# Kernel tuning notes

Measured on AMD Instinct MI355X. Metric: run time of the kernel, lower is better.

## Reference

```python
import jax, jax.numpy as jnp
import numpy as np

N_P = 100000; N_F = 100000; N_PORT = 50000
F_IN = 64; H = 128; E = 200000; G = 128; OUT = 2


def setup_inputs() -> dict:
    key = jax.random.key(0)
    it = iter(jax.random.split(key, 64))
    def nrm(sh, s=1.0):
        return jax.random.normal(next(it), sh, jnp.float32) * s
    def ei(ns, nd):
        src = jax.random.randint(next(it), (E,), 0, ns)
        dst = jax.random.randint(next(it), (E,), 0, nd)
        return jnp.stack([src, dst]).astype(jnp.int32)
    def batch(n):
        return jnp.sort(jax.random.randint(next(it), (n,), 0, G)).astype(jnp.int32)
    return {
        'x_process': nrm((N_P, F_IN)), 'x_file': nrm((N_F, F_IN)), 'x_port': nrm((N_PORT, F_IN)),
        'W0': nrm((F_IN, H), 0.1), 'a0s': nrm((H,), 0.1), 'a0d': nrm((H,), 0.1), 'b0': jnp.zeros((H,), jnp.float32),
        'W1': nrm((H, H), 0.1), 'a1s': nrm((H,), 0.1), 'a1d': nrm((H,), 0.1), 'b1': jnp.zeros((H,), jnp.float32),
        'W2': nrm((H, H), 0.1), 'a2s': nrm((H,), 0.1), 'a2d': nrm((H,), 0.1), 'b2': jnp.zeros((H,), jnp.float32),
        'lin1_w': nrm((H, H), 0.1), 'lin1_b': jnp.zeros((H,), jnp.float32),
        'lin2_w': nrm((H, OUT), 0.1), 'lin2_b': jnp.zeros((OUT,), jnp.float32),
        'ei_access': ei(N_P, N_F), 'ei_rev_access': ei(N_F, N_P),
        'ei_same_as': ei(N_P, N_F), 'ei_rev_same_as': ei(N_F, N_P),
        'ei_bind': ei(N_P, N_PORT), 'ei_rev_bind': ei(N_PORT, N_P),
        'ei_session': ei(N_PORT, N_PORT), 'ei_rev_session': ei(N_PORT, N_PORT),
        'ei_create': ei(N_P, N_P), 'ei_rev_create': ei(N_P, N_P),
        'batch_process': batch(N_P), 'batch_file': batch(N_F), 'batch_port': batch(N_PORT),
    }


def _rel(h_src, s_src, d_dst, ei, b, n_dst):
    # single GATConv relation: gather, segment-softmax over dst, scatter-sum
    es, ed = ei[0], ei[1]
    alpha = jax.nn.leaky_relu(s_src[es] + d_dst[ed], 0.2)  # [E]
    m = jax.ops.segment_max(alpha, ed, num_segments=n_dst)
    m = jnp.where(jnp.isfinite(m), m, 0.0)
    ex = jnp.exp(alpha - m[ed])
    den = jax.ops.segment_sum(ex, ed, num_segments=n_dst)
    w = ex / jnp.maximum(den[ed], 1e-16)
    out = jax.ops.segment_sum(w[:, None] * h_src[es], ed, num_segments=n_dst)
    return out + b


def _forward(x_process, x_file, x_port,
             W0, a0s, a0d, b0, W1, a1s, a1d, b1, W2, a2s, a2d, b2,
             lin1_w, lin1_b, lin2_w, lin2_b,
             ei_access, ei_rev_access, ei_same_as, ei_rev_same_as,
             ei_bind, ei_rev_bind, ei_session, ei_rev_session,
             ei_create, ei_rev_create,
             batch_process, batch_file, batch_port):
    xp, xf, xpo = x_process, x_file, x_port
    for W, asr, adr, b in ((W0, a0s, a0d, b0), (W1, a1s, a1d, b1), (W2, a2s, a2d, b2)):
        # shared GATConv weights across all 10 relations -> transform each node type once
        hp, hf, hpo = xp @ W, xf @ W, xpo @ W
        sp, sf, spo = hp @ asr, hf @ asr, hpo @ asr
        dp, df, dpo = hp @ adr, hf @ adr, hpo @ adr
        # HeteroConv(aggr='mean'): average relation outputs per dst node type
        p_new = (_rel(hf, sf, dp, ei_rev_access, b, N_P)
                 + _rel(hf, sf, dp, ei_rev_same_as, b, N_P)
                 + _rel(hpo, spo, dp, ei_rev_bind, b, N_P)
                 + _rel(hp, sp, dp, ei_create, b, N_P)
                 + _rel(hp, sp, dp, ei_rev_create, b, N_P)) / 5.0
        f_new = (_rel(hp, sp, df, ei_access, b, N_F)
                 + _rel(hp, sp, df, ei_same_as, b, N_F)) / 2.0
        po_new = (_rel(hp, sp, dpo, ei_bind, b, N_PORT)
                  + _rel(hpo, spo, dpo, ei_session, b, N_PORT)
                  + _rel(hpo, spo, dpo, ei_rev_session, b, N_PORT)) / 3.0
        xp = jax.nn.leaky_relu(p_new, 0.01)
        xf = jax.nn.leaky_relu(f_new, 0.01)
        xpo = jax.nn.leaky_relu(po_new, 0.01)
    # pool_type == 1: global_add_pool over all node types concatenated
    x = jnp.concatenate([xp, xf, xpo], axis=0)
    bb = jnp.concatenate([batch_process, batch_file, batch_port], axis=0)
    pooled = jax.ops.segment_sum(x, bb, num_segments=G)  # [G, H]
    h = pooled @ lin1_w + lin1_b  # dropout is identity at eval
    return h @ lin2_w + lin2_b  # [G, OUT]


def reference(x_process, x_file, x_port,
              W0, a0s, a0d, b0, W1, a1s, a1d, b1, W2, a2s, a2d, b2,
              lin1_w, lin1_b, lin2_w, lin2_b,
              ei_access, ei_rev_access, ei_same_as, ei_rev_same_as,
              ei_bind, ei_rev_bind, ei_session, ei_rev_session,
              ei_create, ei_rev_create,
              batch_process, batch_file, batch_port):
    return _forward(x_process, x_file, x_port,
                    W0, a0s, a0d, b0, W1, a1s, a1d, b1, W2, a2s, a2d, b2,
                    lin1_w, lin1_b, lin2_w, lin2_b,
                    ei_access, ei_rev_access, ei_same_as, ei_rev_same_as,
                    ei_bind, ei_rev_bind, ei_session, ei_rev_session,
                    ei_create, ei_rev_create,
                    batch_process, batch_file, batch_port)
```

## Files before the change

### kernel.cpp

```cpp
#include <hip/hip_runtime.h>
#include <cstdint>
#include <cstddef>

#define E_EDGES 200000
#define NP 100000
#define NF 100000
#define NPORT 50000
#define NTOT 250000
#define TOTDEG 850000
#define GPOOL 128

typedef __attribute__((ext_vector_type(8))) short bf16x8;
typedef __attribute__((ext_vector_type(4))) float f32x4;

__device__ __forceinline__ float bf2f(unsigned short u) {
    return __uint_as_float(((unsigned int)u) << 16);
}
__device__ __forceinline__ unsigned short f2bf(float f) {
    unsigned int x = __float_as_uint(f);
    return (unsigned short)((x + 0x7fffu + ((x >> 16) & 1u)) >> 16);
}

struct EiPtrs {
    const int* p[10];
};

__device__ __forceinline__ int seg_of(int r, int dst) {
    if (r < 5) return dst * 5 + r;
    if (r < 7) return 500000 + dst * 2 + (r - 5);
    return 700000 + dst * 3 + (r - 7);
}
__device__ __forceinline__ int srcbase_of(int r) {
    return (r <= 1) ? 100000 : (r == 2 || r >= 8) ? 200000 : 0;
}

__global__ __launch_bounds__(256) void k_count_all(EiPtrs eis, int* __restrict__ deg) {
    int r = blockIdx.y;
    int e = blockIdx.x * 256 + threadIdx.x;
    if (e >= E_EDGES) return;
    atomicAdd(&deg[seg_of(r, eis.p[r][E_EDGES + e])], 1);
}

__global__ __launch_bounds__(256) void k_scan_partial(const int* __restrict__ deg,
                                                      int* __restrict__ bsum) {
    int t = threadIdx.x, b = blockIdx.x;
    int base = b * 1024 + t * 4;
    int sv = 0;
#pragma unroll
    for (int i = 0; i < 4; i++) {
        int idx = base + i;
        if (idx < TOTDEG) sv += deg[idx];
    }
#pragma unroll
    for (int msk = 1; msk < 64; msk <<= 1) sv += __shfl_xor(sv, msk);
    __shared__ int ws[4];
    if ((t & 63) == 0) ws[t >> 6] = sv;
    __syncthreads();
    if (t == 0) bsum[b] = ws[0] + ws[1] + ws[2] + ws[3];
}

__global__ __launch_bounds__(1024) void k_scan_bsums(int* __restrict__ bsum, int nb) {
    __shared__ int lds[1024];
    int t = threadIdx.x;
    int v = (t < nb) ? bsum[t] : 0;
    lds[t] = v;
    __syncthreads();
    for (int dd = 1; dd < 1024; dd <<= 1) {
        int u = (t >= dd) ? lds[t - dd] : 0;
        __syncthreads();
        lds[t] += u;
        __syncthreads();
    }
    if (t < nb) bsum[t] = lds[t] - v;
}

__global__ __launch_bounds__(256) void k_scan_final(const int* __restrict__ deg,
                                                    const int* __restrict__ bsum,
                                                    int* __restrict__ offs) {
    int t = threadIdx.x, b = blockIdx.x;
    int base = b * 1024 + t * 4;
    int v[4];
    int tot = 0;
#pragma unroll
    for (int i = 0; i < 4; i++) {
        int idx = base + i;
        v[i] = (idx < TOTDEG) ? deg[idx] : 0;
        tot += v[i];
    }
    int lane = t & 63, w = t >> 6;
    int x = tot;
#pragma unroll
    for (int dd = 1; dd < 64; dd <<= 1) {
        int u = __shfl_up(x, dd);
        if (lane >= dd) x += u;
    }
    __shared__ int wt[4];
    if (lane == 63) wt[w] = x;
    __syncthreads();
    int wbase = 0;
#pragma unroll
    for (int j = 0; j < 4; j++)
        if (j < w) wbase += wt[j];
    int run = bsum[b] + wbase + (x - tot);
#pragma unroll
    for (int i = 0; i < 4; i++) {
        int idx = base + i;
        if (idx <= TOTDEG) offs[idx] = run;
        run += v[i];
    }
}

__global__ __launch_bounds__(256) void k_fill_all(EiPtrs eis, const int* __restrict__ offs,
                                                  int* __restrict__ cursor,
                                                  int* __restrict__ list) {
    int r = blockIdx.y;
    int e = blockIdx.x * 256 + threadIdx.x;
    if (e >= E_EDGES) return;
    const int* ei = eis.p[r];
    int seg = seg_of(r, ei[E_EDGES + e]);
    int pos = atomicAdd(&cursor[seg], 1);
    list[offs[seg] + pos] = ei[e] + srcbase_of(r);
}

__global__ __launch_bounds__(256) void k_wt(const float* __restrict__ W,
                                            unsigned short* __restrict__ WT, int K) {
    int idx = blockIdx.x * 256 + threadIdx.x;
    if (idx >= 128 * K) return;
    int col = idx / K, k = idx - col * K;
    WT[idx] = f2bf(W[k * 128 + col]);
}

template <int K, bool BF16IN>
__global__ __launch_bounds__(256) void gemm_mfma(const void* __restrict__ xv,
                                                 const unsigned short* __restrict__ WT,
                                                 const float* __restrict__ avs,
                                                 const float* __restrict__ avd,
                                                 unsigned short* __restrict__ h,
                                                 float* __restrict__ s,
                                                 float* __restrict__ d, int N) {
    constexpr int NQ = K / 32;
    __shared__ float csmem[64][130];
    char* sw = (char*)&csmem[0][0];
    int tid = threadIdx.x;
    int w = tid >> 6, l = tid & 63;
    int row0 = blockIdx.x * 64;

    constexpr int WT_BYTES = 128 * K * 2;
#pragma unroll
    for (int i = tid * 16; i < WT_BYTES; i += 256 * 16) {
        uint4 v = *(const uint4*)((const char*)WT + i);
        int row = i / (2 * K);
        int addr = i ^ ((row & 7) << 4);
        *(uint4*)(sw + addr) = v;
    }

    int arow = row0 + w * 16 + (l & 15);
    bf16x8 afrag[NQ];
    if (arow < N) {
        if (BF16IN) {
            const unsigned short* x = (const unsigned short*)xv;
#pragma unroll
            for (int q = 0; q < NQ; ++q) {
                int kc = q * 32 + (l >> 4) * 8;
                afrag[q] = *(const bf16x8*)&x[(size_t)arow * K + kc];
            }
        } else {
            const float* x = (const float*)xv;
#pragma unroll
            for (int q = 0; q < NQ; ++q) {
                int kc = q * 32 + (l >> 4) * 8;
                float4 f0 = *(const float4*)&x[(size_t)arow * K + kc];
                float4 f1 = *(const float4*)&x[(size_t)arow * K + kc + 4];
                bf16x8 a;
                a[0] = (short)f2bf(f0.x);
                a[1] = (short)f2bf(f0.y);
                a[2] = (short)f2bf(f0.z);
                a[3] = (short)f2bf(f0.w);
                a[4] = (short)f2bf(f1.x);
                a[5] = (short)f2bf(f1.y);
                a[6] = (short)f2bf(f1.z);
                a[7] = (short)f2bf(f1.w);
                afrag[q] = a;
            }
        }
    } else {
#pragma unroll
        for (int q = 0; q < NQ; ++q) {
            bf16x8 z = {0, 0, 0, 0, 0, 0, 0, 0};
            afrag[q] = z;
        }
    }
    __syncthreads();

    f32x4 acc[8];
#pragma unroll
    for (int c = 0; c < 8; ++c) acc[c] = (f32x4){0.f, 0.f, 0.f, 0.f};

#pragma unroll
    for (int c = 0; c < 8; ++c) {
        int cabs = c * 16 + (l & 15);
        int base = cabs * (2 * K) + ((l >> 4) * 16);
        int swz = (cabs & 7) << 4;
#pragma unroll
        for (int q = 0; q < NQ; ++q) {
            int addr = (base + q * 64) ^ swz;
            bf16x8 b = *(const bf16x8*)(sw + addr);
            acc[c] = __builtin_amdgcn_mfma_f32_16x16x32_bf16(afrag[q], b, acc[c], 0, 0, 0);
        }
    }
    __syncthreads();

    int crow = w * 16 + (l >> 4) * 4;
    int ccol = l & 15;
#pragma unroll
    for (int c = 0; c < 8; ++c)
#pragma unroll
        for (int r = 0; r < 4; ++r) csmem[crow + r][c * 16 + ccol] = acc[c][r];
    __syncthreads();

    int row = tid >> 2, cg = tid & 3;
    int grow = row0 + row;
    if (grow < N) {
        float sv = 0.f, dv = 0.f;
        unsigned short tmp[32];
#pragma unroll
        for (int i = 0; i < 32; ++i) {
            float v = csmem[row][cg * 32 + i];
            sv = fmaf(v, avs[cg * 32 + i], sv);
            dv = fmaf(v, avd[cg * 32 + i], dv);
            tmp[i] = f2bf(v);
        }
        unsigned short* hp = &h[(size_t)grow * 128 + cg * 32];
        *(uint4*)&hp[0] = *(uint4*)&tmp[0];
        *(uint4*)&hp[8] = *(uint4*)&tmp[8];
        *(uint4*)&hp[16] = *(uint4*)&tmp[16];
        *(uint4*)&hp[24] = *(uint4*)&tmp[24];
        sv += __shfl_xor(sv, 1);
        sv += __shfl_xor(sv, 2);
        dv += __shfl_xor(dv, 1);
        dv += __shfl_xor(dv, 2);
        if (cg == 0) {
            s[grow] = sv;
            d[grow] = dv;
        }
    }
}

__global__ __launch_bounds__(256) void k_edgew(const int* __restrict__ offs,
                                               const int* __restrict__ list,
                                               const float* __restrict__ s_all,
                                               const float* __restrict__ d_all,
                                               unsigned short* __restrict__ wE) {
    int seg = blockIdx.x * 256 + threadIdx.x;
    if (seg >= TOTDEG) return;
    int o0 = offs[seg], o1 = offs[seg + 1];
    if (o1 == o0) return;
    int dst_g;
    if (seg < 500000)
        dst_g = seg / 5;
    else if (seg < 700000)
        dst_g = 100000 + (seg - 500000) / 2;
    else
        dst_g = 200000 + (seg - 700000) / 3;
    float dd = d_all[dst_g];
    float m = -1e30f, den = 0.f;
    for (int j = o0; j < o1; ++j) {
        float x = s_all[list[j]] + dd;
        x = (x >= 0.f) ? x : 0.2f * x;
        if (x > m) {
            den = den * __expf(m - x) + 1.f;
            m = x;
        } else {
            den += __expf(x - m);
        }
    }
    float invden = 1.f / fmaxf(den, 1e-16f);
    for (int j = o0; j < o1; ++j) {
        float x = s_all[list[j]] + dd;
        x = (x >= 0.f) ? x : 0.2f * x;
        wE[j] = f2bf(__expf(x - m) * invden);
    }
}

__global__ __launch_bounds__(256) void k_gather(const int* __restrict__ offs,
                                                const int* __restrict__ list,
                                                const unsigned short* __restrict__ wE,
                                                const float* __restrict__ bias,
                                                const unsigned short* __restrict__ H,
                                                unsigned short* __restrict__ X) {
    int grp = threadIdx.x >> 5, lane = threadIdx.x & 31;
    int dst = blockIdx.x * 8 + grp;
    if (dst >= NTOT) return;
    int seg0, nrel;
    float inv;
    if (dst < 100000) {
        seg0 = dst * 5;
        nrel = 5;
        inv = 0.2f;
    } else if (dst < 200000) {
        seg0 = 500000 + (dst - 100000) * 2;
        nrel = 2;
        inv = 0.5f;
    } else {
        seg0 = 700000 + (dst - 200000) * 3;
        nrel = 3;
        inv = 1.f / 3.f;
    }
    int o0 = offs[seg0], o1 = offs[seg0 + nrel];
    int half = lane >> 4;
    int l16 = lane & 15;
    float a[8] = {0.f, 0.f, 0.f, 0.f, 0.f, 0.f, 0.f, 0.f};
    float b[8] = {0.f, 0.f, 0.f, 0.f, 0.f, 0.f, 0.f, 0.f};
    int j = o0 + half;
    for (; j + 2 < o1; j += 4) {
        int s0 = list[j], s1 = list[j + 2];
        float w0 = bf2f(wE[j]), w1 = bf2f(wE[j + 2]);
        uint4 r0 = *(const uint4*)&H[(size_t)s0 * 128 + l16 * 8];
        uint4 r1 = *(const uint4*)&H[(size_t)s1 * 128 + l16 * 8];
        const unsigned short* u0 = (const unsigned short*)&r0;
        const unsigned short* u1 = (const unsigned short*)&r1;
#pragma unroll
        for (int k = 0; k < 8; ++k) a[k] = fmaf(w0, bf2f(u0[k]), a[k]);
#pragma unroll
        for (int k = 0; k < 8; ++k) b[k] = fmaf(w1, bf2f(u1[k]), b[k]);
    }
    for (; j < o1; j += 2) {
        int s0 = list[j];
        float w0 = bf2f(wE[j]);
        uint4 r0 = *(const uint4*)&H[(size_t)s0 * 128 + l16 * 8];
        const unsigned short* u0 = (const unsigned short*)&r0;
#pragma unroll
        for (int k = 0; k < 8; ++k) a[k] = fmaf(w0, bf2f(u0[k]), a[k]);
    }
#pragma unroll
    for (int k = 0; k < 8; ++k) {
        a[k] += b[k];
        a[k] += __shfl_xor(a[k], 16);
    }
    int c0 = l16 * 8 + half * 4;
    float4 b4 = *(const float4*)&bias[c0];
    float v0 = fmaf(a[half * 4 + 0], inv, b4.x);
    float v1 = fmaf(a[half * 4 + 1], inv, b4.y);
    float v2 = fmaf(a[half * 4 + 2], inv, b4.z);
    float v3 = fmaf(a[half * 4 + 3], inv, b4.w);
    v0 = (v0 >= 0.f) ? v0 : 0.01f * v0;
    v1 = (v1 >= 0.f) ? v1 : 0.01f * v1;
    v2 = (v2 >= 0.f) ? v2 : 0.01f * v2;
    v3 = (v3 >= 0.f) ? v3 : 0.01f * v3;
    ushort4 o;
    o.x = f2bf(v0);
    o.y = f2bf(v1);
    o.z = f2bf(v2);
    o.w = f2bf(v3);
    *(ushort4*)&X[(size_t)dst * 128 + c0] = o;
}

__global__ __launch_bounds__(128) void pool_kernel(const unsigned short* __restrict__ x,
                                                   const int* __restrict__ batch,
                                                   float* __restrict__ pooled, int n) {
    int t = threadIdx.x;
    int start = blockIdx.x * 128;
    int end = min(start + 128, n);
    if (start >= n) return;
    float acc = 0.f;
    int g = batch[start];
    for (int i = start; i < end; ++i) {
        int gi = batch[i];
        if (gi != g) {
            atomicAdd(&pooled[(size_t)g * 128 + t], acc);
            acc = 0.f;
            g = gi;
        }
        acc += bf2f(x[(size_t)i * 128 + t]);
    }
    atomicAdd(&pooled[(size_t)g * 128 + t], acc);
}

__global__ __launch_bounds__(128) void k_mlp(const float* __restrict__ pooled,
                                             const float* __restrict__ w1,
                                             const float* __restrict__ b1,
                                             const float* __restrict__ w2,
                                             const float* __restrict__ b2,
                                             float* __restrict__ out) {
    __shared__ float p[128];
    __shared__ float r0[2], r1[2];
    int g = blockIdx.x, t = threadIdx.x;
    p[t] = pooled[g * 128 + t];
    __syncthreads();
    float acc = b1[t];
    for (int k = 0; k < 128; ++k) acc = fmaf(p[k], w1[k * 128 + t], acc);
    float v0 = acc * w2[t * 2 + 0];
    float v1 = acc * w2[t * 2 + 1];
#pragma unroll
    for (int msk = 1; msk < 64; msk <<= 1) {
        v0 += __shfl_xor(v0, msk);
        v1 += __shfl_xor(v1, msk);
    }
    if ((t & 63) == 0) {
        r0[t >> 6] = v0;
        r1[t >> 6] = v1;
    }
    __syncthreads();
    if (t == 0) {
        out[g * 2 + 0] = r0[0] + r0[1] + b2[0];
        out[g * 2 + 1] = r1[0] + r1[1] + b2[1];
    }
}

__global__ void k_ws_debug(float* out, int n, float val) {
    int i = blockIdx.x * 256 + threadIdx.x;
    if (i < n) out[i] = val;
}

extern "C" void kernel_launch(void* const* d_in, const int* in_sizes, int n_in,
                              void* d_out, int out_size, void* d_ws, size_t ws_size,
                              hipStream_t stream) {
    const float* x_p0 = (const float*)d_in[0];
    const float* x_f0 = (const float*)d_in[1];
    const float* x_po0 = (const float*)d_in[2];
    const float* Wl[3] = {(const float*)d_in[3], (const float*)d_in[7],
                          (const float*)d_in[11]};
    const float* asl[3] = {(const float*)d_in[4], (const float*)d_in[8],
                           (const float*)d_in[12]};
    const float* adl[3] = {(const float*)d_in[5], (const float*)d_in[9],
                           (const float*)d_in[13]};
    const float* bl[3] = {(const float*)d_in[6], (const float*)d_in[10],
                          (const float*)d_in[14]};
    const float* lin1_w = (const float*)d_in[15];
    const float* lin1_b = (const float*)d_in[16];
    const float* lin2_w = (const float*)d_in[17];
    const float* lin2_b = (const float*)d_in[18];
    EiPtrs eis;
    eis.p[0] = (const int*)d_in[20];
    eis.p[1] = (const int*)d_in[22];
    eis.p[2] = (const int*)d_in[24];
    eis.p[3] = (const int*)d_in[27];
    eis.p[4] = (const int*)d_in[28];
    eis.p[5] = (const int*)d_in[19];
    eis.p[6] = (const int*)d_in[21];
    eis.p[7] = (const int*)d_in[23];
    eis.p[8] = (const int*)d_in[25];
    eis.p[9] = (const int*)d_in[26];
    const int* batch_p = (const int*)d_in[29];
    const int* batch_f = (const int*)d_in[30];
    const int* batch_po = (const int*)d_in[31];
    float* out = (float*)d_out;

    char* w = (char*)d_ws;
    size_t off = 0;
    int* offs = (int*)(w + off);      off += (size_t)850004 * 4;
    int* cursor = (int*)(w + off);    off += (size_t)TOTDEG * 4;
    int* list = (int*)(w + off);      off += (size_t)10 * E_EDGES * 4;
    int* bsum = (int*)(w + off);      off += 4096;
    unsigned short* H = (unsigned short*)(w + off); off += (size_t)NTOT * 128 * 2;
    unsigned short* X = (unsigned short*)(w + off); off += (size_t)NTOT * 128 * 2;
    float* s_all = (float*)(w + off); off += (size_t)NTOT * 4;
    float* d_all = (float*)(w + off); off += (size_t)NTOT * 4;
    float* pooled = (float*)(w + off); off += (size_t)GPOOL * 128 * 4;
    unsigned short* WT0 = (unsigned short*)(w + off); off += (size_t)128 * 64 * 2;
    unsigned short* WT1 = (unsigned short*)(w + off); off += (size_t)128 * 128 * 2;
    unsigned short* WT2 = (unsigned short*)(w + off); off += (size_t)128 * 128 * 2;
    unsigned short* wE = (unsigned short*)(w + off); off += (size_t)10 * E_EDGES * 2;
    if (ws_size < off) {
        k_ws_debug<<<(out_size + 255) / 256, 256, 0, stream>>>(out, out_size,
                                                               (float)ws_size);
        return;
    }

    hipMemsetAsync(cursor, 0, (size_t)TOTDEG * 4, stream);
    hipMemsetAsync(pooled, 0, (size_t)GPOOL * 128 * 4, stream);

    k_wt<<<(128 * 64 + 255) / 256, 256, 0, stream>>>(Wl[0], WT0, 64);
    k_wt<<<(128 * 128 + 255) / 256, 256, 0, stream>>>(Wl[1], WT1, 128);
    k_wt<<<(128 * 128 + 255) / 256, 256, 0, stream>>>(Wl[2], WT2, 128);

    int eb = (E_EDGES + 255) / 256;
    k_count_all<<<dim3(eb, 10), 256, 0, stream>>>(eis, cursor);
    int nb = (TOTDEG + 1 + 1023) / 1024;
    k_scan_partial<<<nb, 256, 0, stream>>>(cursor, bsum);
    k_scan_bsums<<<1, 1024, 0, stream>>>(bsum, nb);
    k_scan_final<<<nb, 256, 0, stream>>>(cursor, bsum, offs);
    hipMemsetAsync(cursor, 0, (size_t)TOTDEG * 4, stream);
    k_fill_all<<<dim3(eb, 10), 256, 0, stream>>>(eis, offs, cursor, list);

    unsigned short* Hp = H;
    unsigned short* Hf = H + (size_t)NP * 128;
    unsigned short* Hpo = H + (size_t)(NP + NF) * 128;
    float* sp_ = s_all;
    float* sf_ = s_all + NP;
    float* spo_ = s_all + NP + NF;
    float* dp_ = d_all;
    float* df_ = d_all + NP;
    float* dpo_ = d_all + NP + NF;

    for (int L = 0; L < 3; ++L) {
        if (L == 0) {
            gemm_mfma<64, false><<<(NP + 63) / 64, 256, 0, stream>>>(
                x_p0, WT0, asl[0], adl[0], Hp, sp_, dp_, NP);
            gemm_mfma<64, false><<<(NF + 63) / 64, 256, 0, stream>>>(
                x_f0, WT0, asl[0], adl[0], Hf, sf_, df_, NF);
            gemm_mfma<64, false><<<(NPORT + 63) / 64, 256, 0, stream>>>(
                x_po0, WT0, asl[0], adl[0], Hpo, spo_, dpo_, NPORT);
        } else {
            const unsigned short* WTL = (L == 1) ? WT1 : WT2;
            gemm_mfma<128, true><<<(NTOT + 63) / 64, 256, 0, stream>>>(
                X, WTL, asl[L], adl[L], H, s_all, d_all, NTOT);
        }
        k_edgew<<<(TOTDEG + 255) / 256, 256, 0, stream>>>(offs, list, s_all, d_all, wE);
        k_gather<<<(NTOT + 7) / 8, 256, 0, stream>>>(offs, list, wE, bl[L], H, X);
    }

    unsigned short* Xp = X;
    unsigned short* Xf = X + (size_t)NP * 128;
    unsigned short* Xpo = X + (size_t)(NP + NF) * 128;
    pool_kernel<<<(NP + 127) / 128, 128, 0, stream>>>(Xp, batch_p, pooled, NP);
    pool_kernel<<<(NF + 127) / 128, 128, 0, stream>>>(Xf, batch_f, pooled, NF);
    pool_kernel<<<(NPORT + 127) / 128, 128, 0, stream>>>(Xpo, batch_po, pooled, NPORT);

    k_mlp<<<GPOOL, 128, 0, stream>>>(pooled, lin1_w, lin1_b, lin2_w, lin2_b, out);
}
```

Measured before the change: 901.3 us.

## Partition CSR count/fill atomics by segment range and merge pool launches

The count and fill kernels gain a third grid dimension of 8 partitions, and each partition only does atomics for segments in its range, so concurrently active atomics touch a smaller address window and should localize in cache. The fill now starts its cursor from a copy of the offsets, so the atomic directly returns the final list position and the separate offs lookup is dropped. The three pooling launches are merged into one kernel over all node types. In exchange, every edge index is read 8 times and the grid is 8x larger.

```diff
diff --git a/kernel.cpp b/kernel.cpp
--- a/kernel.cpp
+++ b/kernel.cpp
@@ -9,6 +9,8 @@
 #define NTOT 250000
 #define TOTDEG 850000
 #define GPOOL 128
+#define NPART 8
+#define SEGS_PER_PART 106250
 
 typedef __attribute__((ext_vector_type(8))) short bf16x8;
 typedef __attribute__((ext_vector_type(4))) float f32x4;
@@ -38,7 +40,10 @@
     int r = blockIdx.y;
     int e = blockIdx.x * 256 + threadIdx.x;
     if (e >= E_EDGES) return;
-    atomicAdd(&deg[seg_of(r, eis.p[r][E_EDGES + e])], 1);
+    int seg = seg_of(r, eis.p[r][E_EDGES + e]);
+    int lo = blockIdx.z * SEGS_PER_PART;
+    if (seg < lo || seg >= lo + SEGS_PER_PART) return;
+    atomicAdd(&deg[seg], 1);
 }
 
 __global__ __launch_bounds__(256) void k_scan_partial(const int* __restrict__ deg,
@@ -110,16 +115,17 @@
     }
 }
 
-__global__ __launch_bounds__(256) void k_fill_all(EiPtrs eis, const int* __restrict__ offs,
-                                                  int* __restrict__ cursor,
+__global__ __launch_bounds__(256) void k_fill_all(EiPtrs eis, int* __restrict__ cursor,
                                                   int* __restrict__ list) {
     int r = blockIdx.y;
     int e = blockIdx.x * 256 + threadIdx.x;
     if (e >= E_EDGES) return;
     const int* ei = eis.p[r];
     int seg = seg_of(r, ei[E_EDGES + e]);
+    int lo = blockIdx.z * SEGS_PER_PART;
+    if (seg < lo || seg >= lo + SEGS_PER_PART) return;
     int pos = atomicAdd(&cursor[seg], 1);
-    list[offs[seg] + pos] = ei[e] + srcbase_of(r);
+    list[pos] = ei[e] + srcbase_of(r);
 }
 
 __global__ __launch_bounds__(256) void k_wt(const float* __restrict__ W,
@@ -355,23 +361,28 @@
     *(ushort4*)&X[(size_t)dst * 128 + c0] = o;
 }
 
-__global__ __launch_bounds__(128) void pool_kernel(const unsigned short* __restrict__ x,
-                                                   const int* __restrict__ batch,
-                                                   float* __restrict__ pooled, int n) {
+__global__ __launch_bounds__(128) void pool_all(const unsigned short* __restrict__ X,
+                                                const int* __restrict__ bp,
+                                                const int* __restrict__ bf,
+                                                const int* __restrict__ bpo,
+                                                float* __restrict__ pooled) {
     int t = threadIdx.x;
     int start = blockIdx.x * 128;
-    int end = min(start + 128, n);
-    if (start >= n) return;
+    int end = min(start + 128, NTOT);
+    if (start >= end) return;
+    auto bat = [&](int i) {
+        return (i < NP) ? bp[i] : (i < NP + NF) ? bf[i - NP] : bpo[i - NP - NF];
+    };
     float acc = 0.f;
-    int g = batch[start];
+    int g = bat(start);
     for (int i = start; i < end; ++i) {
-        int gi = batch[i];
+        int gi = bat(i);
         if (gi != g) {
             atomicAdd(&pooled[(size_t)g * 128 + t], acc);
             acc = 0.f;
             g = gi;
         }
-        acc += bf2f(x[(size_t)i * 128 + t]);
+        acc += bf2f(X[(size_t)i * 128 + t]);
     }
     atomicAdd(&pooled[(size_t)g * 128 + t], acc);
 }
@@ -475,13 +486,13 @@
     k_wt<<<(128 * 128 + 255) / 256, 256, 0, stream>>>(Wl[2], WT2, 128);
 
     int eb = (E_EDGES + 255) / 256;
-    k_count_all<<<dim3(eb, 10), 256, 0, stream>>>(eis, cursor);
+    k_count_all<<<dim3(eb, 10, NPART), 256, 0, stream>>>(eis, cursor);
     int nb = (TOTDEG + 1 + 1023) / 1024;
     k_scan_partial<<<nb, 256, 0, stream>>>(cursor, bsum);
     k_scan_bsums<<<1, 1024, 0, stream>>>(bsum, nb);
     k_scan_final<<<nb, 256, 0, stream>>>(cursor, bsum, offs);
-    hipMemsetAsync(cursor, 0, (size_t)TOTDEG * 4, stream);
-    k_fill_all<<<dim3(eb, 10), 256, 0, stream>>>(eis, offs, cursor, list);
+    hipMemcpyAsync(cursor, offs, (size_t)TOTDEG * 4, hipMemcpyDeviceToDevice, stream);
+    k_fill_all<<<dim3(eb, 10, NPART), 256, 0, stream>>>(eis, cursor, list);
 
     unsigned short* Hp = H;
     unsigned short* Hf = H + (size_t)NP * 128;
@@ -510,12 +521,8 @@
         k_gather<<<(NTOT + 7) / 8, 256, 0, stream>>>(offs, list, wE, bl[L], H, X);
     }
 
-    unsigned short* Xp = X;
-    unsigned short* Xf = X + (size_t)NP * 128;
-    unsigned short* Xpo = X + (size_t)(NP + NF) * 128;
-    pool_kernel<<<(NP + 127) / 128, 128, 0, stream>>>(Xp, batch_p, pooled, NP);
-    pool_kernel<<<(NF + 127) / 128, 128, 0, stream>>>(Xf, batch_f, pooled, NF);
-    pool_kernel<<<(NPORT + 127) / 128, 128, 0, stream>>>(Xpo, batch_po, pooled, NPORT);
+    pool_all<<<(NTOT + 127) / 128, 128, 0, stream>>>(X, batch_p, batch_f, batch_po,
+                                                     pooled);
 
     k_mlp<<<GPOOL, 128, 0, stream>>>(pooled, lin1_w, lin1_b, lin2_w, lin2_b, out);
 }
```

Measured after the change: 862.8 us. 1.04x faster.
